# Optimization experiments

Hardware: AMD Instinct MI355X
Metric: run time of the kernel (lower is better)

## Reference

```python
import jax, jax.numpy as jnp
import numpy as np

B, N, C = 4, 1024, 1024
H, D = 16, 64            # n_heads, head_dim; inner_dim = H*D = C
L = 6                    # n_blocks
FF = 4 * C
SCALE = C ** (-0.5)      # source uses width**-0.5
EPS = 1e-5


def setup_inputs() -> dict:
    key = jax.random.key(0)
    ks = jax.random.split(key, 9)
    s = 0.02
    return {
        "x":     jax.random.normal(ks[0], (B, N, C), dtype=jnp.float32),
        "Wqkv":  jax.random.normal(ks[1], (L, C, 3 * H * D), dtype=jnp.float32) * s,
        "Wout":  jax.random.normal(ks[2], (L, H * D, C), dtype=jnp.float32) * s,
        "bout":  jnp.zeros((L, C), dtype=jnp.float32),
        "W1":    jax.random.normal(ks[3], (L, C, FF), dtype=jnp.float32) * s,
        "b1":    jnp.zeros((L, FF), dtype=jnp.float32),
        "W2":    jax.random.normal(ks[4], (L, FF, C), dtype=jnp.float32) * s,
        "b2":    jnp.zeros((L, C), dtype=jnp.float32),
        "ln1_g": jnp.ones((C,), dtype=jnp.float32),
        "ln1_b": jnp.zeros((C,), dtype=jnp.float32),
        "ln2_g": jnp.ones((C,), dtype=jnp.float32),
        "ln2_b": jnp.zeros((C,), dtype=jnp.float32),
    }


def _layernorm(y, g, b):
    mu = jnp.mean(y, axis=-1, keepdims=True)
    var = jnp.mean(jnp.square(y - mu), axis=-1, keepdims=True)
    return (y - mu) * jax.lax.rsqrt(var + EPS) * g + b


def reference(x, Wqkv, Wout, bout, W1, b1, W2, b2, ln1_g, ln1_b, ln2_g, ln2_b):
    for l in range(L):
        # --- pre-norm multi-head attention (shared LN params across blocks) ---
        h = _layernorm(x, ln1_g, ln1_b)
        qkv = h @ Wqkv[l]                              # [B,N,3HD]
        q, k, v = jnp.split(qkv, 3, axis=-1)
        def heads(t):
            return t.reshape(B, N, H, D).transpose(0, 2, 1, 3)  # [B,H,N,D]
        q, k, v = heads(q), heads(k), heads(v)
        dots = jnp.einsum('bhid,bhjd->bhij', q, k) * SCALE
        attn = jax.nn.softmax(dots, axis=-1)
        o = jnp.einsum('bhij,bhjd->bhid', attn, v)     # [B,H,N,D]
        o = o.transpose(0, 2, 1, 3).reshape(B, N, H * D)
        x = x + (o @ Wout[l] + bout[l])
        # --- pre-norm FFN with exact GELU ---
        h2 = _layernorm(x, ln2_g, ln2_b)
        f = jax.nn.gelu(h2 @ W1[l] + b1[l], approximate=False) @ W2[l] + b2[l]
        x = x + f
    return x
```

## Files before the change

### kernel.cpp

```cpp
#include <hip/hip_runtime.h>
#include <stdint.h>

typedef unsigned short u16;
typedef __bf16  bf16x8 __attribute__((ext_vector_type(8)));
typedef float   f32x4  __attribute__((ext_vector_type(4)));

#define DEVINL __device__ __forceinline__

DEVINL u16 f2bf(float f) {
    union { float f; uint32_t u; } v; v.f = f;
    uint32_t r = v.u + 0x7fffu + ((v.u >> 16) & 1u);
    return (u16)(r >> 16);
}

DEVINL float gelu_exact(float x) {
    return 0.5f * x * (1.0f + erff(x * 0.70710678118654752f));
}

typedef const void __attribute__((address_space(1))) gvoid;
typedef void __attribute__((address_space(3))) lvoid;
DEVINL void gload_lds16(const u16* g, u16* l) {
    __builtin_amdgcn_global_load_lds((gvoid*)g, (lvoid*)l, 16, 0, 0);
}

__global__ __launch_bounds__(256) void k_transpose_conv(
    const float* __restrict__ W, u16* __restrict__ Wt, int K, int N) {
    __shared__ float t[32][33];
    const int n0 = blockIdx.x * 32, k0 = blockIdx.y * 32;
    const int tx = threadIdx.x & 31, ty = threadIdx.x >> 5;
#pragma unroll
    for (int i = 0; i < 4; i++)
        t[ty + i * 8][tx] = W[(size_t)(k0 + ty + i * 8) * N + n0 + tx];
    __syncthreads();
#pragma unroll
    for (int i = 0; i < 4; i++)
        Wt[(size_t)(n0 + ty + i * 8) * K + k0 + tx] = f2bf(t[tx][ty + i * 8]);
}

__global__ __launch_bounds__(256) void k_layernorm(
    const float* __restrict__ x, const float* __restrict__ g,
    const float* __restrict__ b, u16* __restrict__ out) {
    const int row = blockIdx.x, tid = threadIdx.x;
    float4 v = ((const float4*)x)[(size_t)row * 256 + tid];
    float s  = v.x + v.y + v.z + v.w;
    float s2 = v.x * v.x + v.y * v.y + v.z * v.z + v.w * v.w;
#pragma unroll
    for (int off = 32; off > 0; off >>= 1) {
        s  += __shfl_down(s, off);
        s2 += __shfl_down(s2, off);
    }
    __shared__ float rs[4], rs2[4];
    const int wv = tid >> 6;
    if ((tid & 63) == 0) { rs[wv] = s; rs2[wv] = s2; }
    __syncthreads();
    s  = rs[0] + rs[1] + rs[2] + rs[3];
    s2 = rs2[0] + rs2[1] + rs2[2] + rs2[3];
    const float mu  = s * (1.0f / 1024.0f);
    const float var = s2 * (1.0f / 1024.0f) - mu * mu;
    const float rstd = rsqrtf(var + 1e-5f);
    float4 gv = ((const float4*)g)[tid];
    float4 bv = ((const float4*)b)[tid];
    uint2 o;
    u16 a0 = f2bf((v.x - mu) * rstd * gv.x + bv.x);
    u16 a1 = f2bf((v.y - mu) * rstd * gv.y + bv.y);
    u16 a2 = f2bf((v.z - mu) * rstd * gv.z + bv.z);
    u16 a3 = f2bf((v.w - mu) * rstd * gv.w + bv.w);
    o.x = a0 | ((uint32_t)a1 << 16);
    o.y = a2 | ((uint32_t)a3 << 16);
    ((uint2*)out)[(size_t)row * 256 + tid] = o;
}

enum { EPI_BF16 = 0, EPI_F32_ATOMIC = 1, EPI_BF16_BIAS_GELU = 2 };

template <int EPI>
__global__ __launch_bounds__(256) void k_gemm_bt(
    const u16* __restrict__ A, const u16* __restrict__ Bt,
    void* outp, const float* __restrict__ bias,
    int N, int K, int kPer) {
    __shared__ __align__(16) u16 As[128 * 32];
    __shared__ __align__(16) u16 Bs[128 * 32];
    const int tid  = threadIdx.x;
    const int lane = tid & 63, wv = tid >> 6;
    const int wm = wv >> 1, wn = wv & 1;
    const int lr = lane >> 2;
    const int lc = ((lane & 3) ^ ((lane >> 3) & 3)) * 8;
    const int c0 = wv * 2;
    const size_t aRow0 = (size_t)blockIdx.y * 128;
    const size_t bRow0 = (size_t)blockIdx.x * 128;
    const int ks = blockIdx.z;
    const int kBase = ks * kPer;

    f32x4 acc[4][4] = {};
    const int mrow = lane & 15;
    const int quad = lane >> 4;
    const int koff = ((quad ^ ((mrow >> 1) & 3)) << 3);
    const int kIters = kPer >> 5;

    for (int kt = 0; kt < kIters; kt++) {
        const int k0 = kBase + (kt << 5);
        gload_lds16(A  + (aRow0 + (size_t)(c0 * 16      + lr)) * K + k0 + lc, &As[c0 * 512]);
        gload_lds16(A  + (aRow0 + (size_t)(c0 * 16 + 16 + lr)) * K + k0 + lc, &As[(c0 + 1) * 512]);
        gload_lds16(Bt + (bRow0 + (size_t)(c0 * 16      + lr)) * K + k0 + lc, &Bs[c0 * 512]);
        gload_lds16(Bt + (bRow0 + (size_t)(c0 * 16 + 16 + lr)) * K + k0 + lc, &Bs[(c0 + 1) * 512]);
        __syncthreads();
        bf16x8 af[4], bfv[4];
#pragma unroll
        for (int i = 0; i < 4; i++)
            af[i] = *(const bf16x8*)&As[(wm * 64 + i * 16 + mrow) * 32 + koff];
#pragma unroll
        for (int i = 0; i < 4; i++)
            bfv[i] = *(const bf16x8*)&Bs[(wn * 64 + i * 16 + mrow) * 32 + koff];
#pragma unroll
        for (int mi = 0; mi < 4; mi++)
#pragma unroll
            for (int ni = 0; ni < 4; ni++)
                acc[mi][ni] = __builtin_amdgcn_mfma_f32_16x16x32_bf16(
                    af[mi], bfv[ni], acc[mi][ni], 0, 0, 0);
        __syncthreads();
    }

    const int rr = quad * 4;
    const int cc = mrow;
#pragma unroll
    for (int mi = 0; mi < 4; mi++) {
#pragma unroll
        for (int ni = 0; ni < 4; ni++) {
#pragma unroll
            for (int r = 0; r < 4; r++) {
                const size_t row = aRow0 + wm * 64 + mi * 16 + rr + r;
                const size_t col = bRow0 + wn * 64 + ni * 16 + cc;
                const float v = acc[mi][ni][r];
                if (EPI == EPI_BF16) {
                    ((u16*)outp)[row * N + col] = f2bf(v);
                } else if (EPI == EPI_F32_ATOMIC) {
                    const float add = (ks == 0) ? v + bias[col] : v;
                    atomicAdd(&((float*)outp)[row * N + col], add);
                } else {
                    ((u16*)outp)[row * N + col] = f2bf(gelu_exact(v + bias[col]));
                }
            }
        }
    }
}

__global__ __launch_bounds__(256) void k_vtrans(
    const u16* __restrict__ qkv, u16* __restrict__ vT) {
    __shared__ u16 t[32][33];
    const int bh = blockIdx.z;
    const int b = bh >> 4, h = bh & 15;
    const int n0 = blockIdx.x * 32, d0 = blockIdx.y * 32;
    const int tx = threadIdx.x & 31, ty = threadIdx.x >> 5;
#pragma unroll
    for (int i = 0; i < 4; i++)
        t[ty + i * 8][tx] = qkv[(size_t)(b * 1024 + n0 + ty + i * 8) * 3072 + 2048 + h * 64 + d0 + tx];
    __syncthreads();
#pragma unroll
    for (int i = 0; i < 4; i++)
        vT[(size_t)(bh * 64 + d0 + ty + i * 8) * 1024 + n0 + tx] = t[tx][ty + i * 8];
}

__global__ __launch_bounds__(256) void k_attention(
    const u16* __restrict__ qkv, const u16* __restrict__ vT, u16* __restrict__ o) {
    const int qt = blockIdx.x, h = blockIdx.y, b = blockIdx.z;
    const int tid = threadIdx.x;
    const int lane = tid & 63, wv = tid >> 6;
    const int quad = lane >> 4, l16 = lane & 15;
    __shared__ __align__(16) u16 Ks[64 * 64];
    __shared__ __align__(16) u16 Vs[64 * 64];
    __shared__ __align__(16) u16 Ps[4][16 * 72];
    const int q0 = qt * 64 + wv * 16;

    bf16x8 qa[2];
    {
        const u16* qp = qkv + (size_t)(b * 1024 + q0 + l16) * 3072 + h * 64 + quad * 8;
        qa[0] = *(const bf16x8*)qp;
        qa[1] = *(const bf16x8*)(qp + 32);
    }
    f32x4 oacc[4] = {};
    float mst[4], lst[4];
#pragma unroll
    for (int r = 0; r < 4; r++) { mst[r] = -__builtin_inff(); lst[r] = 0.f; }

    const int tr = tid >> 3, tc = tid & 7;
    const int cs = (tc ^ (tr & 7)) * 8;
    const size_t kvbase = (size_t)(b * 1024) * 3072 + 1024 + h * 64;
    const size_t vtbase = (size_t)(b * 16 + h) * 64 * 1024;

    for (int j0 = 0; j0 < 1024; j0 += 64) {
        *(uint4*)&Ks[tr * 64 + cs]        = *(const uint4*)&qkv[kvbase + (size_t)(j0 + tr) * 3072 + tc * 8];
        *(uint4*)&Ks[(tr + 32) * 64 + cs] = *(const uint4*)&qkv[kvbase + (size_t)(j0 + tr + 32) * 3072 + tc * 8];
        *(uint4*)&Vs[tr * 64 + cs]        = *(const uint4*)&vT[vtbase + (size_t)tr * 1024 + j0 + tc * 8];
        *(uint4*)&Vs[(tr + 32) * 64 + cs] = *(const uint4*)&vT[vtbase + (size_t)(tr + 32) * 1024 + j0 + tc * 8];
        __syncthreads();

        f32x4 s[4] = {};
#pragma unroll
        for (int nt = 0; nt < 4; nt++) {
            const int rk = nt * 16 + l16;
            bf16x8 kb0 = *(const bf16x8*)&Ks[rk * 64 + ((quad ^ (rk & 7)) * 8)];
            bf16x8 kb1 = *(const bf16x8*)&Ks[rk * 64 + (((quad + 4) ^ (rk & 7)) * 8)];
            s[nt] = __builtin_amdgcn_mfma_f32_16x16x32_bf16(qa[0], kb0, s[nt], 0, 0, 0);
            s[nt] = __builtin_amdgcn_mfma_f32_16x16x32_bf16(qa[1], kb1, s[nt], 0, 0, 0);
        }
#pragma unroll
        for (int r = 0; r < 4; r++) {
            float v0 = s[0][r] * 0.03125f, v1 = s[1][r] * 0.03125f;
            float v2 = s[2][r] * 0.03125f, v3 = s[3][r] * 0.03125f;
            float mx = fmaxf(fmaxf(v0, v1), fmaxf(v2, v3));
#pragma unroll
            for (int off = 1; off < 16; off <<= 1) mx = fmaxf(mx, __shfl_xor(mx, off));
            const float mnew = fmaxf(mst[r], mx);
            const float alpha = __expf(mst[r] - mnew);
            mst[r] = mnew;
            const float p0 = __expf(v0 - mnew), p1 = __expf(v1 - mnew);
            const float p2 = __expf(v2 - mnew), p3 = __expf(v3 - mnew);
            float rsum = p0 + p1 + p2 + p3;
#pragma unroll
            for (int off = 1; off < 16; off <<= 1) rsum += __shfl_xor(rsum, off);
            lst[r] = lst[r] * alpha + rsum;
#pragma unroll
            for (int dt = 0; dt < 4; dt++) oacc[dt][r] *= alpha;
            u16* pr = &Ps[wv][(quad * 4 + r) * 72 + l16];
            pr[0]  = f2bf(p0); pr[16] = f2bf(p1);
            pr[32] = f2bf(p2); pr[48] = f2bf(p3);
        }
        __syncthreads();
        bf16x8 pa0 = *(const bf16x8*)&Ps[wv][l16 * 72 + quad * 8];
        bf16x8 pa1 = *(const bf16x8*)&Ps[wv][l16 * 72 + quad * 8 + 32];
#pragma unroll
        for (int dt = 0; dt < 4; dt++) {
            const int rv = dt * 16 + l16;
            bf16x8 vb0 = *(const bf16x8*)&Vs[rv * 64 + ((quad ^ (rv & 7)) * 8)];
            bf16x8 vb1 = *(const bf16x8*)&Vs[rv * 64 + (((quad + 4) ^ (rv & 7)) * 8)];
            oacc[dt] = __builtin_amdgcn_mfma_f32_16x16x32_bf16(pa0, vb0, oacc[dt], 0, 0, 0);
            oacc[dt] = __builtin_amdgcn_mfma_f32_16x16x32_bf16(pa1, vb1, oacc[dt], 0, 0, 0);
        }
        __syncthreads();
    }
#pragma unroll
    for (int dt = 0; dt < 4; dt++)
#pragma unroll
        for (int r = 0; r < 4; r++) {
            const float v = oacc[dt][r] / lst[r];
            o[(size_t)(b * 1024 + q0 + quad * 4 + r) * 1024 + h * 64 + dt * 16 + l16] = f2bf(v);
        }
}

extern "C" void kernel_launch(void* const* d_in, const int* in_sizes, int n_in,
                              void* d_out, int out_size, void* d_ws, size_t ws_size,
                              hipStream_t stream) {
    const float* x_in = (const float*)d_in[0];
    const float* Wqkv = (const float*)d_in[1];
    const float* Wout = (const float*)d_in[2];
    const float* bout = (const float*)d_in[3];
    const float* W1   = (const float*)d_in[4];
    const float* b1   = (const float*)d_in[5];
    const float* W2   = (const float*)d_in[6];
    const float* b2   = (const float*)d_in[7];
    const float* ln1g = (const float*)d_in[8];
    const float* ln1b = (const float*)d_in[9];
    const float* ln2g = (const float*)d_in[10];
    const float* ln2b = (const float*)d_in[11];
    float* xbuf = (float*)d_out;

    char* p = (char*)d_ws;
    auto carve = [&](size_t elems) -> u16* {
        u16* r = (u16*)p;
        p += ((elems * 2 + 255) & ~(size_t)255);
        return r;
    };
    u16* wq   = carve((size_t)3072 * 1024);
    u16* wo   = carve((size_t)1024 * 1024);
    u16* w1t  = carve((size_t)4096 * 1024);
    u16* w2t  = carve((size_t)1024 * 4096);
    u16* hb   = carve((size_t)4096 * 1024);
    u16* qkvb = carve((size_t)4096 * 3072);
    u16* vtb  = carve((size_t)4096 * 1024);
    u16* ob   = carve((size_t)4096 * 1024);
    u16* gb   = carve((size_t)4096 * 4096);
    if ((size_t)(p - (char*)d_ws) > ws_size) return;

    hipMemcpyAsync(xbuf, x_in, (size_t)4096 * 1024 * 4, hipMemcpyDeviceToDevice, stream);

    for (int l = 0; l < 6; l++) {
        k_transpose_conv<<<dim3(96, 32), 256, 0, stream>>>(Wqkv + (size_t)l * 1024 * 3072, wq, 1024, 3072);
        k_transpose_conv<<<dim3(32, 32), 256, 0, stream>>>(Wout + (size_t)l * 1024 * 1024, wo, 1024, 1024);
        k_transpose_conv<<<dim3(128, 32), 256, 0, stream>>>(W1 + (size_t)l * 1024 * 4096, w1t, 1024, 4096);
        k_transpose_conv<<<dim3(32, 128), 256, 0, stream>>>(W2 + (size_t)l * 4096 * 1024, w2t, 4096, 1024);

        k_layernorm<<<4096, 256, 0, stream>>>(xbuf, ln1g, ln1b, hb);
        k_gemm_bt<EPI_BF16><<<dim3(24, 32, 1), 256, 0, stream>>>(hb, wq, qkvb, nullptr, 3072, 1024, 1024);
        k_vtrans<<<dim3(32, 2, 64), 256, 0, stream>>>(qkvb, vtb);
        k_attention<<<dim3(16, 16, 4), 256, 0, stream>>>(qkvb, vtb, ob);
        k_gemm_bt<EPI_F32_ATOMIC><<<dim3(8, 32, 2), 256, 0, stream>>>(ob, wo, xbuf, bout + (size_t)l * 1024, 1024, 1024, 512);
        k_layernorm<<<4096, 256, 0, stream>>>(xbuf, ln2g, ln2b, hb);
        k_gemm_bt<EPI_BF16_BIAS_GELU><<<dim3(32, 32, 1), 256, 0, stream>>>(hb, w1t, gb, b1 + (size_t)l * 4096, 4096, 1024, 1024);
        k_gemm_bt<EPI_F32_ATOMIC><<<dim3(8, 32, 4), 256, 0, stream>>>(gb, w2t, xbuf, b2 + (size_t)l * 1024, 1024, 4096, 1024);
    }
}
```

Before: 2.256 ms.

## Double-buffer GEMM LDS tiles and drop split-K atomics for out-projection

Measured after the change: 2.041 ms. 9.5% less time.

```diff
diff --git a/kernel.cpp b/kernel.cpp
--- a/kernel.cpp
+++ b/kernel.cpp
@@ -70,15 +70,15 @@
     ((uint2*)out)[(size_t)row * 256 + tid] = o;
 }
 
-enum { EPI_BF16 = 0, EPI_F32_ATOMIC = 1, EPI_BF16_BIAS_GELU = 2 };
+enum { EPI_BF16 = 0, EPI_F32_ATOMIC = 1, EPI_BF16_BIAS_GELU = 2, EPI_F32_BIAS_RES = 3 };
 
 template <int EPI>
 __global__ __launch_bounds__(256) void k_gemm_bt(
     const u16* __restrict__ A, const u16* __restrict__ Bt,
-    void* outp, const float* __restrict__ bias,
+    void* outp, const float* __restrict__ bias, const float* __restrict__ res,
     int N, int K, int kPer) {
-    __shared__ __align__(16) u16 As[128 * 32];
-    __shared__ __align__(16) u16 Bs[128 * 32];
+    __shared__ __align__(16) u16 As[2][128 * 32];
+    __shared__ __align__(16) u16 Bs[2][128 * 32];
     const int tid  = threadIdx.x;
     const int lane = tid & 63, wv = tid >> 6;
     const int wm = wv >> 1, wn = wv & 1;
@@ -96,27 +96,41 @@
     const int koff = ((quad ^ ((mrow >> 1) & 3)) << 3);
     const int kIters = kPer >> 5;
 
+    const u16* aP = A  + (aRow0 + (size_t)(c0 * 16 + lr)) * K + kBase + lc;
+    const u16* bP = Bt + (bRow0 + (size_t)(c0 * 16 + lr)) * K + kBase + lc;
+    const size_t rowStep = (size_t)16 * K;
+
+    gload_lds16(aP,           &As[0][c0 * 512]);
+    gload_lds16(aP + rowStep, &As[0][(c0 + 1) * 512]);
+    gload_lds16(bP,           &Bs[0][c0 * 512]);
+    gload_lds16(bP + rowStep, &Bs[0][(c0 + 1) * 512]);
+
     for (int kt = 0; kt < kIters; kt++) {
-        const int k0 = kBase + (kt << 5);
-        gload_lds16(A  + (aRow0 + (size_t)(c0 * 16      + lr)) * K + k0 + lc, &As[c0 * 512]);
-        gload_lds16(A  + (aRow0 + (size_t)(c0 * 16 + 16 + lr)) * K + k0 + lc, &As[(c0 + 1) * 512]);
-        gload_lds16(Bt + (bRow0 + (size_t)(c0 * 16      + lr)) * K + k0 + lc, &Bs[c0 * 512]);
-        gload_lds16(Bt + (bRow0 + (size_t)(c0 * 16 + 16 + lr)) * K + k0 + lc, &Bs[(c0 + 1) * 512]);
-        __syncthreads();
+        const int buf = kt & 1;
+        if (kt + 1 < kIters) {
+            const int k0 = (kt + 1) << 5;
+            gload_lds16(aP + k0,           &As[buf ^ 1][c0 * 512]);
+            gload_lds16(aP + k0 + rowStep, &As[buf ^ 1][(c0 + 1) * 512]);
+            gload_lds16(bP + k0,           &Bs[buf ^ 1][c0 * 512]);
+            gload_lds16(bP + k0 + rowStep, &Bs[buf ^ 1][(c0 + 1) * 512]);
+            asm volatile("s_waitcnt vmcnt(4)\n\ts_barrier" ::: "memory");
+        } else {
+            asm volatile("s_waitcnt vmcnt(0)\n\ts_barrier" ::: "memory");
+        }
         bf16x8 af[4], bfv[4];
 #pragma unroll
         for (int i = 0; i < 4; i++)
-            af[i] = *(const bf16x8*)&As[(wm * 64 + i * 16 + mrow) * 32 + koff];
+            af[i] = *(const bf16x8*)&As[buf][(wm * 64 + i * 16 + mrow) * 32 + koff];
 #pragma unroll
         for (int i = 0; i < 4; i++)
-            bfv[i] = *(const bf16x8*)&Bs[(wn * 64 + i * 16 + mrow) * 32 + koff];
+            bfv[i] = *(const bf16x8*)&Bs[buf][(wn * 64 + i * 16 + mrow) * 32 + koff];
 #pragma unroll
         for (int mi = 0; mi < 4; mi++)
 #pragma unroll
             for (int ni = 0; ni < 4; ni++)
                 acc[mi][ni] = __builtin_amdgcn_mfma_f32_16x16x32_bf16(
                     af[mi], bfv[ni], acc[mi][ni], 0, 0, 0);
-        __syncthreads();
+        asm volatile("s_barrier" ::: "memory");
     }
 
     const int rr = quad * 4;
@@ -135,6 +149,8 @@
                 } else if (EPI == EPI_F32_ATOMIC) {
                     const float add = (ks == 0) ? v + bias[col] : v;
                     atomicAdd(&((float*)outp)[row * N + col], add);
+                } else if (EPI == EPI_F32_BIAS_RES) {
+                    ((float*)outp)[row * N + col] = res[row * N + col] + v + bias[col];
                 } else {
                     ((u16*)outp)[row * N + col] = f2bf(gelu_exact(v + bias[col]));
                 }
@@ -289,12 +305,12 @@
         k_transpose_conv<<<dim3(32, 128), 256, 0, stream>>>(W2 + (size_t)l * 4096 * 1024, w2t, 4096, 1024);
 
         k_layernorm<<<4096, 256, 0, stream>>>(xbuf, ln1g, ln1b, hb);
-        k_gemm_bt<EPI_BF16><<<dim3(24, 32, 1), 256, 0, stream>>>(hb, wq, qkvb, nullptr, 3072, 1024, 1024);
+        k_gemm_bt<EPI_BF16><<<dim3(24, 32, 1), 256, 0, stream>>>(hb, wq, qkvb, nullptr, nullptr, 3072, 1024, 1024);
         k_vtrans<<<dim3(32, 2, 64), 256, 0, stream>>>(qkvb, vtb);
         k_attention<<<dim3(16, 16, 4), 256, 0, stream>>>(qkvb, vtb, ob);
-        k_gemm_bt<EPI_F32_ATOMIC><<<dim3(8, 32, 2), 256, 0, stream>>>(ob, wo, xbuf, bout + (size_t)l * 1024, 1024, 1024, 512);
+        k_gemm_bt<EPI_F32_BIAS_RES><<<dim3(8, 32, 1), 256, 0, stream>>>(ob, wo, xbuf, bout + (size_t)l * 1024, xbuf, 1024, 1024, 1024);
         k_layernorm<<<4096, 256, 0, stream>>>(xbuf, ln2g, ln2b, hb);
-        k_gemm_bt<EPI_BF16_BIAS_GELU><<<dim3(32, 32, 1), 256, 0, stream>>>(hb, w1t, gb, b1 + (size_t)l * 4096, 4096, 1024, 1024);
-        k_gemm_bt<EPI_F32_ATOMIC><<<dim3(8, 32, 4), 256, 0, stream>>>(gb, w2t, xbuf, b2 + (size_t)l * 1024, 1024, 4096, 1024);
-    }
-}
+        k_gemm_bt<EPI_BF16_BIAS_GELU><<<dim3(32, 32, 1), 256, 0, stream>>>(hb, w1t, gb, b1 + (size_t)l * 4096, nullptr, 4096, 1024, 1024);
+        k_gemm_bt<EPI_F32_ATOMIC><<<dim3(8, 32, 2), 256, 0, stream>>>(gb, w2t, xbuf, b2 + (size_t)l * 1024, nullptr, 1024, 4096, 2048);
+    }
+}
```
